# Kernel optimization log

Hardware: AMD Instinct MI355X
Metric: run time of the kernel (lower is better)

## Reference

```python
import jax, jax.numpy as jnp
import numpy as np

NEG = -1e10  # the original uses -10000000000.0
B, T, L = 64, 512, 64
START, END = 0, L - 1


def setup_inputs() -> dict:
    key = jax.random.key(0)
    k_em, k_tr, k_len = jax.random.split(key, 3)
    emission_scores = jax.random.normal(k_em, (B, T, L), dtype=jnp.float32)
    # transition initialized as in __init__: randn with start column / end row masked
    transition = jax.random.normal(k_tr, (L, L), dtype=jnp.float32)
    transition = transition.at[:, START].set(NEG)
    transition = transition.at[END, :].set(NEG)
    sent_lens = jax.random.randint(k_len, (B,), T // 2, T + 1, dtype=jnp.int32)
    return {"emission_scores": emission_scores, "transition": transition,
            "sent_lens": sent_lens}


def reference(emission_scores, transition, sent_lens):
    # --- calculate_all_scores ---
    em = emission_scores.at[:, :, START].set(NEG).at[:, :, END].set(NEG)
    # scores[b,t,y_prev,y_t] = transition[y_prev,y_t] + emission[b,t,y_t]
    scores = transition[None, None, :, :] + em[:, :, None, :]  # [B,T,L,L]
    scores = scores.at[:, 1:, START, :].set(NEG)

    # --- forward_score: sequential DP via scan ---
    alpha0 = scores[:, 0, START, :]  # [B,L]

    def step(alpha_prev, s_t):  # s_t: [B,L,L]
        alpha_t = jax.nn.logsumexp(alpha_prev[:, :, None] + s_t, axis=1)
        return alpha_t, alpha_t

    _, alphas_rest = jax.lax.scan(step, alpha0, jnp.moveaxis(scores[:, 1:], 1, 0))
    alpha = jnp.concatenate([alpha0[:, None, :], jnp.moveaxis(alphas_rest, 0, 1)],
                            axis=1)  # [B,T,L]

    idx = (sent_lens - 1).astype(jnp.int32)[:, None, None]  # [B,1,1]
    last_alpha = jnp.take_along_axis(alpha, idx, axis=1)[:, 0, :]  # [B,L]
    last_alpha = last_alpha + transition[:, END][None, :]
    log_Z = jax.nn.logsumexp(last_alpha, axis=1)  # [B]
    return alpha, log_Z
```

## Files before the change

kernel.cpp:

```cpp
#include <hip/hip_runtime.h>

#define NEGV -10000000000.0f
constexpr int Bn = 64, Tn = 512, Ln = 64;
constexpr int CK = 32;
constexpr int NC = 16;
constexpr int QP = 68;

typedef float f32x16 __attribute__((ext_vector_type(16)));
typedef __bf16 bf16x8 __attribute__((ext_vector_type(8)));
typedef unsigned int u32;
typedef unsigned short u16;

__device__ inline float waveMaxF(float v) {
#pragma unroll
    for (int off = 32; off > 0; off >>= 1)
        v = fmaxf(v, __shfl_xor(v, off, 64));
    return v;
}
__device__ inline u32 packbf(float a, float b) {
    u32 ua = __float_as_uint(a) + 0x8000u;
    u32 ub = __float_as_uint(b) + 0x8000u;
    return (ua >> 16) | (ub & 0xffff0000u);
}
__device__ inline float lo16f(u32 d) { return __uint_as_float(d << 16); }
__device__ inline float hi16f(u32 d) { return __uint_as_float(d & 0xffff0000u); }

template <bool FIRST>
__device__ void chunk_scan(const float* __restrict__ emb, const float* __restrict__ tr,
                           float* __restrict__ outb, float* uLDS,
                           const float* Ecol,
                           float entry,
                           int t0, int j, int len, float* aLastOut, float trSj) {
    const bool edge = (j == 0) || (j == Ln - 1);
    float emq[4];
#pragma unroll
    for (int tt = 0; tt < 4; ++tt) {
        float v = emb[(t0 + tt) * Ln + j];
        emq[tt] = edge ? NEGV : v;
    }
    float aPrev, mPrev, u;
    int tauStart;
    if (FIRST) {
        float a0 = trSj + emq[0];
        outb[t0 * Ln + j] = a0;
        aPrev = a0;
        mPrev = __shfl(a0, 1, 64);
        u = __expf(a0 - mPrev);
        tauStart = 1;
    } else {
        aPrev = entry;
        mPrev = __shfl(entry, 1, 64);
        u = __expf(entry - mPrev);
        tauStart = 0;
    }
    float aLast = *aLastOut;
#pragma unroll 4
    for (int tau = tauStart; tau < CK; ++tau) {
        const int t = t0 + tau;
        uLDS[j] = u;
        const float em_t = emq[tau & 3];
        const int tp = tau + 4;
        if (tp < CK) {
            float v = emb[(t0 + tp) * Ln + j];
            emq[tp & 3] = edge ? NEGV : v;
        }
        float mNext = __shfl(aPrev, 1, 64);
        float cf = __expf(em_t + (mPrev - mNext));
        float acc0 = 0.f, acc1 = 0.f, acc2 = 0.f, acc3 = 0.f;
        const float4* u4 = reinterpret_cast<const float4*>(uLDS);
#pragma unroll
        for (int i4 = 0; i4 < 16; ++i4) {
            float4 uv = u4[i4];
            acc0 = fmaf(uv.x, Ecol[4 * i4 + 0], acc0);
            acc1 = fmaf(uv.y, Ecol[4 * i4 + 1], acc1);
            acc2 = fmaf(uv.z, Ecol[4 * i4 + 2], acc2);
            acc3 = fmaf(uv.w, Ecol[4 * i4 + 3], acc3);
        }
        float S = (acc0 + acc1) + (acc2 + acc3);
        float lg = __logf(S);
        lg = (S > 0.f) ? lg : NEGV;
        float a_t = em_t + (mPrev + lg);
        outb[t * Ln + j] = a_t;
        if (t == len - 1) aLast = a_t;
        u = S * cf;
        aPrev = a_t;
        mPrev = mNext;
    }
    *aLastOut = aLast;
    uLDS[j] = aPrev;
}

__global__ __launch_bounds__(64) void crf_passA(const float* __restrict__ em,
                                                const float* __restrict__ tr,
                                                float* __restrict__ out,
                                                float* __restrict__ wsE,
                                                float* __restrict__ wsS) {
    const int b = blockIdx.x & 63;
    const int cix = blockIdx.x >> 6;
    const int L = threadIdx.x;
    __shared__ alignas(16) float gtab[CK * 64];
    __shared__ alignas(16) u16 Qlds[64 * QP];
    __shared__ alignas(16) float uLDS[64];

    if (cix == 0) {
        float Ecol[Ln];
#pragma unroll
        for (int i = 0; i < Ln; ++i) Ecol[i] = __expf(tr[i * Ln + L]);
        const float trSj = tr[L];
        const float* emb = em + (size_t)b * Tn * Ln;
        float* outb = out + (size_t)b * Tn * Ln;
        float dummyLast = 0.f;
        chunk_scan<true>(emb, tr, outb, uLDS, Ecol, 0.f, 0, L,  -12345, &dummyLast, trSj);
        wsE[b * 1024 + 1 * 64 + L] = uLDS[L];
        return;
    }

    const int t0 = CK * cix;
    const int h = L >> 5;
    const int c31 = L & 31;

    float sSum = 0.f;
#pragma unroll 4
    for (int tau = 0; tau < CK; ++tau) {
        float v = em[((size_t)b * Tn + (t0 + tau)) * Ln + L];
        if (L == 0 || L == Ln - 1) v = NEGV;
        float s = waveMaxF(v);
        gtab[tau * 64 + L] = __expf(v - s);
        sSum += s;
    }

    uint4 Ap[2][4];
#pragma unroll
    for (int I = 0; I < 2; ++I)
#pragma unroll
        for (int kc = 0; kc < 4; ++kc) {
            float e[8];
#pragma unroll
            for (int q = 0; q < 8; ++q) {
                int k = 16 * kc + 8 * h + q;
                e[q] = __expf(tr[k * Ln + 32 * I + c31]);
            }
            Ap[I][kc] = make_uint4(packbf(e[0], e[1]), packbf(e[2], e[3]),
                                   packbf(e[4], e[5]), packbf(e[6], e[7]));
        }

    float mxPrev;
    {
        float mx0 = 0.f;
#pragma unroll
        for (int k4 = 0; k4 < 16; ++k4) {
            float v0 = __expf(tr[L * Ln + 4 * k4 + 0]) * gtab[4 * k4 + 0];
            float v1 = __expf(tr[L * Ln + 4 * k4 + 1]) * gtab[4 * k4 + 1];
            float v2 = __expf(tr[L * Ln + 4 * k4 + 2]) * gtab[4 * k4 + 2];
            float v3 = __expf(tr[L * Ln + 4 * k4 + 3]) * gtab[4 * k4 + 3];
            mx0 = fmaxf(mx0, fmaxf(fmaxf(v0, v1), fmaxf(v2, v3)));
            uint2 w;
            w.x = packbf(v0, v1);
            w.y = packbf(v2, v3);
            *(uint2*)&Qlds[L * QP + 4 * k4] = w;
        }
        mxPrev = waveMaxF(mx0);
    }
    float sigma = sSum;
    const f32x16 Z = (f32x16)(0.0f);

    for (int tau = 1; tau < CK; ++tau) {
        uint4 Bp[2][4];
#pragma unroll
        for (int J = 0; J < 2; ++J)
#pragma unroll
            for (int kc = 0; kc < 4; ++kc) {
                const u16* p = &Qlds[(32 * J + c31) * QP + 16 * kc + 8 * h];
                uint2 q0 = *(const uint2*)(p);
                uint2 q1 = *(const uint2*)(p + 4);
                Bp[J][kc] = make_uint4(q0.x, q0.y, q1.x, q1.y);
            }
        f32x16 acc[2][2];
#pragma unroll
        for (int I = 0; I < 2; ++I)
#pragma unroll
            for (int J = 0; J < 2; ++J) {
                f32x16 a = Z;
#pragma unroll
                for (int kc = 0; kc < 4; ++kc)
                    a = __builtin_amdgcn_mfma_f32_32x32x16_bf16(
                        __builtin_bit_cast(bf16x8, Ap[I][kc]),
                        __builtin_bit_cast(bf16x8, Bp[J][kc]), a, 0, 0, 0);
                acc[I][J] = a;
            }
        float rho = 1.0f / mxPrev;
        sigma += __logf(mxPrev);
        float nmx = 0.f;
#pragma unroll
        for (int I = 0; I < 2; ++I)
#pragma unroll
            for (int rg = 0; rg < 4; ++rg) {
                int k0 = 32 * I + 8 * rg + 4 * h;
                float4 G = *(const float4*)&gtab[tau * 64 + k0];
                float g0 = G.x * rho, g1 = G.y * rho, g2 = G.z * rho, g3 = G.w * rho;
#pragma unroll
                for (int J = 0; J < 2; ++J) {
                    float v0 = acc[I][J][4 * rg + 0] * g0;
                    float v1 = acc[I][J][4 * rg + 1] * g1;
                    float v2 = acc[I][J][4 * rg + 2] * g2;
                    float v3 = acc[I][J][4 * rg + 3] * g3;
                    nmx = fmaxf(nmx, fmaxf(fmaxf(v0, v1), fmaxf(v2, v3)));
                    uint2 w;
                    w.x = packbf(v0, v1);
                    w.y = packbf(v2, v3);
                    *(uint2*)&Qlds[(32 * J + c31) * QP + k0] = w;
                }
            }
        mxPrev = waveMaxF(nmx);
    }

    {
        float rv[64];
        float rmax = 0.f;
#pragma unroll
        for (int n = 0; n < 64; ++n) {
            float v = __uint_as_float(((u32)Qlds[n * QP + L]) << 16);
            rv[n] = v;
            rmax = fmaxf(rmax, v);
        }
        float inv = (rmax > 0.f) ? 1.0f / rmax : 0.f;
        float sj = (rmax > 0.f) ? sigma + __logf(rmax) : 0.f;
        u32* og = (u32*)out + (size_t)b * (Tn * Ln) + (size_t)cix * (CK * Ln) + L * 32;
#pragma unroll
        for (int w8 = 0; w8 < 8; ++w8) {
            uint4 w;
            w.x = packbf(rv[8 * w8 + 0] * inv, rv[8 * w8 + 1] * inv);
            w.y = packbf(rv[8 * w8 + 2] * inv, rv[8 * w8 + 3] * inv);
            w.z = packbf(rv[8 * w8 + 4] * inv, rv[8 * w8 + 5] * inv);
            w.w = packbf(rv[8 * w8 + 6] * inv, rv[8 * w8 + 7] * inv);
            *(uint4*)(og + 4 * w8) = w;
        }
        wsS[b * 1024 + cix * 64 + L] = sj;
    }
}

__global__ __launch_bounds__(64) void crf_passB(const float* __restrict__ out,
                                                float* __restrict__ wsE,
                                                const float* __restrict__ wsS) {
    const int b = blockIdx.x;
    const int j = threadIdx.x;
    __shared__ alignas(16) float uL[64];
    const u32* Qbase = (const u32*)out + (size_t)b * (Tn * Ln);

    float e = wsE[b * 1024 + 1 * 64 + j];
    uint4 nxt[8];
    float signxt = wsS[b * 1024 + 1 * 64 + j];
#pragma unroll
    for (int r = 0; r < 8; ++r) nxt[r] = *(const uint4*)(Qbase + 1 * (CK * Ln) + j * 32 + 4 * r);

#pragma unroll
    for (int c = 1; c <= 14; ++c) {
        uint4 cur[8];
#pragma unroll
        for (int r = 0; r < 8; ++r) cur[r] = nxt[r];
        float sig = signxt;
        if (c < 14) {
#pragma unroll
            for (int r = 0; r < 8; ++r)
                nxt[r] = *(const uint4*)(Qbase + (size_t)(c + 1) * (CK * Ln) + j * 32 + 4 * r);
            signxt = wsS[b * 1024 + (c + 1) * 64 + j];
        }
        float m = __shfl(e, 1, 64);
        uL[j] = __expf(e - m);
        const float4* u4 = reinterpret_cast<const float4*>(uL);
        float S = 0.f;
#pragma unroll
        for (int i4 = 0; i4 < 16; ++i4) {
            float4 uv = u4[i4];
            u32 d0 = ((const u32*)cur)[2 * i4];
            u32 d1 = ((const u32*)cur)[2 * i4 + 1];
            S = fmaf(uv.x, lo16f(d0), S);
            S = fmaf(uv.y, hi16f(d0), S);
            S = fmaf(uv.z, lo16f(d1), S);
            S = fmaf(uv.w, hi16f(d1), S);
        }
        float a;
        if (S > 0.f) a = m + sig + __logf(S);
        else a = m + NEGV + ((j == 0) ? NEGV : 0.f);
        e = a;
        wsE[b * 1024 + (c + 1) * 64 + j] = e;
    }
}

__global__ __launch_bounds__(64) void crf_passC(const float* __restrict__ em,
                                                const float* __restrict__ tr,
                                                const int* __restrict__ lens,
                                                float* __restrict__ out,
                                                const float* __restrict__ wsE) {
    const int b = blockIdx.x & 63;
    const int cix = 1 + (blockIdx.x >> 6);
    const int j = threadIdx.x;
    __shared__ alignas(16) float uLDS[64];

    float Ecol[Ln];
#pragma unroll
    for (int i = 0; i < Ln; ++i) Ecol[i] = __expf(tr[i * Ln + j]);
    const float trEj = tr[j * Ln + (Ln - 1)];
    const int len = lens[b];
    const float* emb = em + (size_t)b * Tn * Ln;
    float* outb = out + (size_t)b * Tn * Ln;
    const float entry = wsE[b * 1024 + cix * 64 + j];

    float aLast = 0.f;
    chunk_scan<false>(emb, tr, outb, uLDS, Ecol, entry, CK * cix, j, len, &aLast, 0.f);

    if (((len - 1) >> 5) == cix) {
        float last = aLast + trEj;
        float m2 = last;
#pragma unroll
        for (int off = 32; off > 0; off >>= 1)
            m2 = fmaxf(m2, __shfl_xor(m2, off, 64));
        float e2 = __expf(last - m2);
#pragma unroll
        for (int off = 32; off > 0; off >>= 1)
            e2 += __shfl_xor(e2, off, 64);
        if (j == 0) out[(size_t)Bn * Tn * Ln + b] = m2 + __logf(e2);
    }
}

__global__ __launch_bounds__(64) void crf_fallback(const float* __restrict__ em,
                                                   const float* __restrict__ tr,
                                                   const int* __restrict__ lens,
                                                   float* __restrict__ out) {
    const int b = blockIdx.x;
    const int j = threadIdx.x;
    __shared__ alignas(16) float uLDS[Ln];
    float E[Ln];
#pragma unroll
    for (int i = 0; i < Ln; ++i) E[i] = __expf(tr[i * Ln + j]);
    const float trSj = tr[j];
    const float trEj = tr[j * Ln + (Ln - 1)];
    const int len = lens[b];
    const bool edge = (j == 0) || (j == Ln - 1);
    const float* emb = em + (size_t)b * Tn * Ln;
    float* outb = out + (size_t)b * Tn * Ln;
    float emq[4];
#pragma unroll
    for (int tt = 0; tt < 4; ++tt) {
        float v = emb[tt * Ln + j];
        emq[tt] = edge ? NEGV : v;
    }
    float a = trSj + emq[0];
    outb[j] = a;
    float aPrev = a, aLast = a;
    float mPrev = __shfl(a, 1, 64);
    float u = __expf(a - mPrev);
#pragma unroll 4
    for (int t = 1; t < Tn; ++t) {
        uLDS[j] = u;
        const float em_t = emq[t & 3];
        const int tp = t + 4;
        if (tp < Tn) {
            float v = emb[tp * Ln + j];
            emq[tp & 3] = edge ? NEGV : v;
        }
        float mNext = __shfl(aPrev, 1, 64);
        float cf = __expf(em_t + (mPrev - mNext));
        float acc0 = 0.f, acc1 = 0.f, acc2 = 0.f, acc3 = 0.f;
        const float4* u4 = reinterpret_cast<const float4*>(uLDS);
#pragma unroll
        for (int i4 = 0; i4 < 16; ++i4) {
            float4 uv = u4[i4];
            acc0 = fmaf(uv.x, E[4 * i4 + 0], acc0);
            acc1 = fmaf(uv.y, E[4 * i4 + 1], acc1);
            acc2 = fmaf(uv.z, E[4 * i4 + 2], acc2);
            acc3 = fmaf(uv.w, E[4 * i4 + 3], acc3);
        }
        float S = (acc0 + acc1) + (acc2 + acc3);
        float lg = __logf(S);
        lg = (S > 0.f) ? lg : NEGV;
        float a_t = em_t + (mPrev + lg);
        outb[t * Ln + j] = a_t;
        if (t == len - 1) aLast = a_t;
        u = S * cf;
        aPrev = a_t;
        mPrev = mNext;
    }
    float last = aLast + trEj;
    float m2 = last;
#pragma unroll
    for (int off = 32; off > 0; off >>= 1)
        m2 = fmaxf(m2, __shfl_xor(m2, off, 64));
    float e2 = __expf(last - m2);
#pragma unroll
    for (int off = 32; off > 0; off >>= 1)
        e2 += __shfl_xor(e2, off, 64);
    if (j == 0) out[(size_t)Bn * Tn * Ln + b] = m2 + __logf(e2);
}

extern "C" void kernel_launch(void* const* d_in, const int* in_sizes, int n_in,
                              void* d_out, int out_size, void* d_ws, size_t ws_size,
                              hipStream_t stream) {
    const float* em = (const float*)d_in[0];
    const float* tr = (const float*)d_in[1];
    const int* lens = (const int*)d_in[2];
    float* out = (float*)d_out;
    const size_t wsNeed = 2u * 64 * 16 * 64 * sizeof(float);
    if (ws_size >= wsNeed) {
        float* wsE = (float*)d_ws;
        float* wsS = wsE + 64 * 16 * 64;
        crf_passA<<<dim3(1024), dim3(64), 0, stream>>>(em, tr, out, wsE, wsS);
        crf_passB<<<dim3(64), dim3(64), 0, stream>>>(out, wsE, wsS);
        crf_passC<<<dim3(960), dim3(64), 0, stream>>>(em, tr, lens, out, wsE);
    } else {
        crf_fallback<<<dim3(Bn), dim3(64), 0, stream>>>(em, tr, lens, out);
    }
}
```

Before: 143.3 us.

## Split passA chunk matrix product across two waves with lazy rescaling

crf_passA now runs with 128 threads. Each wave owns one 32-column half of the chunk transfer matrix, so each wave issues half the MFMAs per step and the serial chain per block gets shorter. The per-timestep wave max and renormalization now run only every fourth step, with separate per-wave scale accumulators reconciled at the end through LDS. The emission max reductions are batched across 16 timesteps to expose more ILP. The cost is an extra wave per block, two barriers, and a risk of bf16 range growth between rescales.

```diff
diff --git a/kernel.cpp b/kernel.cpp
--- a/kernel.cpp
+++ b/kernel.cpp
@@ -26,11 +26,10 @@
 __device__ inline float hi16f(u32 d) { return __uint_as_float(d & 0xffff0000u); }
 
 template <bool FIRST>
-__device__ void chunk_scan(const float* __restrict__ emb, const float* __restrict__ tr,
+__device__ void chunk_scan(const float* __restrict__ emb,
                            float* __restrict__ outb, float* uLDS,
-                           const float* Ecol,
-                           float entry,
-                           int t0, int j, int len, float* aLastOut, float trSj) {
+                           const float* Ecol, float entry, int t0, int j, int len,
+                           float trSj, float* aLastOut, float* aFinalOut) {
     const bool edge = (j == 0) || (j == Ln - 1);
     float emq[4];
 #pragma unroll
@@ -87,47 +86,68 @@
         mPrev = mNext;
     }
     *aLastOut = aLast;
-    uLDS[j] = aPrev;
-}
-
-__global__ __launch_bounds__(64) void crf_passA(const float* __restrict__ em,
-                                                const float* __restrict__ tr,
-                                                float* __restrict__ out,
-                                                float* __restrict__ wsE,
-                                                float* __restrict__ wsS) {
+    *aFinalOut = aPrev;
+}
+
+__global__ __launch_bounds__(128) void crf_passA(const float* __restrict__ em,
+                                                 const float* __restrict__ tr,
+                                                 float* __restrict__ out,
+                                                 float* __restrict__ wsE,
+                                                 float* __restrict__ wsS) {
     const int b = blockIdx.x & 63;
     const int cix = blockIdx.x >> 6;
-    const int L = threadIdx.x;
+    const int J = threadIdx.x >> 6;
+    const int L = threadIdx.x & 63;
     __shared__ alignas(16) float gtab[CK * 64];
     __shared__ alignas(16) u16 Qlds[64 * QP];
     __shared__ alignas(16) float uLDS[64];
+    __shared__ float sLDS[2];
+    __shared__ float sigLDS[2];
 
     if (cix == 0) {
+        if (J == 1) return;
         float Ecol[Ln];
 #pragma unroll
         for (int i = 0; i < Ln; ++i) Ecol[i] = __expf(tr[i * Ln + L]);
         const float trSj = tr[L];
         const float* emb = em + (size_t)b * Tn * Ln;
         float* outb = out + (size_t)b * Tn * Ln;
-        float dummyLast = 0.f;
-        chunk_scan<true>(emb, tr, outb, uLDS, Ecol, 0.f, 0, L,  -12345, &dummyLast, trSj);
-        wsE[b * 1024 + 1 * 64 + L] = uLDS[L];
+        float dummyLast = 0.f, aFinal;
+        chunk_scan<true>(emb, outb, uLDS, Ecol, 0.f, 0, L,  -1, trSj, &dummyLast, &aFinal);
+        wsE[b * 1024 + 1 * 64 + L] = aFinal;
         return;
     }
 
     const int t0 = CK * cix;
+    const int c31 = L & 31;
     const int h = L >> 5;
-    const int c31 = L & 31;
-
-    float sSum = 0.f;
-#pragma unroll 4
-    for (int tau = 0; tau < CK; ++tau) {
-        float v = em[((size_t)b * Tn + (t0 + tau)) * Ln + L];
-        if (L == 0 || L == Ln - 1) v = NEGV;
-        float s = waveMaxF(v);
-        gtab[tau * 64 + L] = __expf(v - s);
-        sSum += s;
-    }
+
+    {
+        float orig[16], sv[16];
+        const int tb = t0 + 16 * J;
+#pragma unroll
+        for (int r = 0; r < 16; ++r) {
+            float v = em[((size_t)b * Tn + (tb + r)) * Ln + L];
+            if (L == 0 || L == Ln - 1) v = NEGV;
+            orig[r] = v;
+            sv[r] = v;
+        }
+#pragma unroll
+        for (int off = 32; off > 0; off >>= 1) {
+#pragma unroll
+            for (int r = 0; r < 16; ++r)
+                sv[r] = fmaxf(sv[r], __shfl_xor(sv[r], off, 64));
+        }
+        float ssum = 0.f;
+#pragma unroll
+        for (int r = 0; r < 16; ++r) {
+            gtab[(16 * J + r) * 64 + L] = __expf(orig[r] - sv[r]);
+            ssum += sv[r];
+        }
+        if (L == 0) sLDS[J] = ssum;
+    }
+    __syncthreads();
+    const float sSum = sLDS[0] + sLDS[1];
 
     uint4 Ap[2][4];
 #pragma unroll
@@ -144,99 +164,101 @@
                                    packbf(e[4], e[5]), packbf(e[6], e[7]));
         }
 
-    float mxPrev;
+    const int n = 32 * J + c31;
     {
-        float mx0 = 0.f;
-#pragma unroll
-        for (int k4 = 0; k4 < 16; ++k4) {
-            float v0 = __expf(tr[L * Ln + 4 * k4 + 0]) * gtab[4 * k4 + 0];
-            float v1 = __expf(tr[L * Ln + 4 * k4 + 1]) * gtab[4 * k4 + 1];
-            float v2 = __expf(tr[L * Ln + 4 * k4 + 2]) * gtab[4 * k4 + 2];
-            float v3 = __expf(tr[L * Ln + 4 * k4 + 3]) * gtab[4 * k4 + 3];
-            mx0 = fmaxf(mx0, fmaxf(fmaxf(v0, v1), fmaxf(v2, v3)));
+        const float* trn = tr + n * Ln + 32 * h;
+        const float* g0 = gtab + 32 * h;
+#pragma unroll
+        for (int k4 = 0; k4 < 8; ++k4) {
+            float v0 = __expf(trn[4 * k4 + 0]) * g0[4 * k4 + 0];
+            float v1 = __expf(trn[4 * k4 + 1]) * g0[4 * k4 + 1];
+            float v2 = __expf(trn[4 * k4 + 2]) * g0[4 * k4 + 2];
+            float v3 = __expf(trn[4 * k4 + 3]) * g0[4 * k4 + 3];
             uint2 w;
             w.x = packbf(v0, v1);
             w.y = packbf(v2, v3);
-            *(uint2*)&Qlds[L * QP + 4 * k4] = w;
-        }
-        mxPrev = waveMaxF(mx0);
-    }
-    float sigma = sSum;
+            *(uint2*)&Qlds[n * QP + 32 * h + 4 * k4] = w;
+        }
+    }
+
+    float sig_w = 0.f;
+    float wm = 1.0f;
     const f32x16 Z = (f32x16)(0.0f);
-
     for (int tau = 1; tau < CK; ++tau) {
-        uint4 Bp[2][4];
-#pragma unroll
-        for (int J = 0; J < 2; ++J)
-#pragma unroll
-            for (int kc = 0; kc < 4; ++kc) {
-                const u16* p = &Qlds[(32 * J + c31) * QP + 16 * kc + 8 * h];
-                uint2 q0 = *(const uint2*)(p);
-                uint2 q1 = *(const uint2*)(p + 4);
-                Bp[J][kc] = make_uint4(q0.x, q0.y, q1.x, q1.y);
+        uint4 Bp[4];
+#pragma unroll
+        for (int kc = 0; kc < 4; ++kc) {
+            const u16* p = &Qlds[n * QP + 16 * kc + 8 * h];
+            uint2 q0 = *(const uint2*)(p);
+            uint2 q1 = *(const uint2*)(p + 4);
+            Bp[kc] = make_uint4(q0.x, q0.y, q1.x, q1.y);
+        }
+        f32x16 acc0 = Z, acc1 = Z;
+#pragma unroll
+        for (int kc = 0; kc < 4; ++kc) {
+            acc0 = __builtin_amdgcn_mfma_f32_32x32x16_bf16(
+                __builtin_bit_cast(bf16x8, Ap[0][kc]),
+                __builtin_bit_cast(bf16x8, Bp[kc]), acc0, 0, 0, 0);
+            acc1 = __builtin_amdgcn_mfma_f32_32x32x16_bf16(
+                __builtin_bit_cast(bf16x8, Ap[1][kc]),
+                __builtin_bit_cast(bf16x8, Bp[kc]), acc1, 0, 0, 0);
+        }
+        const bool doRescale = ((tau & 3) == 0);
+        const bool doMeasure = ((tau & 3) == 2);
+        float rr = 1.0f;
+        if (doRescale) {
+            rr = 1.0f / wm;
+            sig_w += __logf(wm);
+        }
+        float lmax = 0.f;
+#pragma unroll
+        for (int I = 0; I < 2; ++I) {
+#pragma unroll
+            for (int rg = 0; rg < 4; ++rg) {
+                const int k0 = 32 * I + 8 * rg + 4 * h;
+                float4 G = *(const float4*)&gtab[tau * 64 + k0];
+                float v0 = (I ? acc1 : acc0)[4 * rg + 0] * (G.x * rr);
+                float v1 = (I ? acc1 : acc0)[4 * rg + 1] * (G.y * rr);
+                float v2 = (I ? acc1 : acc0)[4 * rg + 2] * (G.z * rr);
+                float v3 = (I ? acc1 : acc0)[4 * rg + 3] * (G.w * rr);
+                if (doMeasure) lmax = fmaxf(lmax, fmaxf(fmaxf(v0, v1), fmaxf(v2, v3)));
+                uint2 w;
+                w.x = packbf(v0, v1);
+                w.y = packbf(v2, v3);
+                *(uint2*)&Qlds[n * QP + k0] = w;
             }
-        f32x16 acc[2][2];
-#pragma unroll
-        for (int I = 0; I < 2; ++I)
-#pragma unroll
-            for (int J = 0; J < 2; ++J) {
-                f32x16 a = Z;
-#pragma unroll
-                for (int kc = 0; kc < 4; ++kc)
-                    a = __builtin_amdgcn_mfma_f32_32x32x16_bf16(
-                        __builtin_bit_cast(bf16x8, Ap[I][kc]),
-                        __builtin_bit_cast(bf16x8, Bp[J][kc]), a, 0, 0, 0);
-                acc[I][J] = a;
-            }
-        float rho = 1.0f / mxPrev;
-        sigma += __logf(mxPrev);
-        float nmx = 0.f;
-#pragma unroll
-        for (int I = 0; I < 2; ++I)
-#pragma unroll
-            for (int rg = 0; rg < 4; ++rg) {
-                int k0 = 32 * I + 8 * rg + 4 * h;
-                float4 G = *(const float4*)&gtab[tau * 64 + k0];
-                float g0 = G.x * rho, g1 = G.y * rho, g2 = G.z * rho, g3 = G.w * rho;
-#pragma unroll
-                for (int J = 0; J < 2; ++J) {
-                    float v0 = acc[I][J][4 * rg + 0] * g0;
-                    float v1 = acc[I][J][4 * rg + 1] * g1;
-                    float v2 = acc[I][J][4 * rg + 2] * g2;
-                    float v3 = acc[I][J][4 * rg + 3] * g3;
-                    nmx = fmaxf(nmx, fmaxf(fmaxf(v0, v1), fmaxf(v2, v3)));
-                    uint2 w;
-                    w.x = packbf(v0, v1);
-                    w.y = packbf(v2, v3);
-                    *(uint2*)&Qlds[(32 * J + c31) * QP + k0] = w;
-                }
-            }
-        mxPrev = waveMaxF(nmx);
-    }
-
-    {
-        float rv[64];
-        float rmax = 0.f;
-#pragma unroll
-        for (int n = 0; n < 64; ++n) {
-            float v = __uint_as_float(((u32)Qlds[n * QP + L]) << 16);
-            rv[n] = v;
-            rmax = fmaxf(rmax, v);
-        }
-        float inv = (rmax > 0.f) ? 1.0f / rmax : 0.f;
-        float sj = (rmax > 0.f) ? sigma + __logf(rmax) : 0.f;
-        u32* og = (u32*)out + (size_t)b * (Tn * Ln) + (size_t)cix * (CK * Ln) + L * 32;
-#pragma unroll
-        for (int w8 = 0; w8 < 8; ++w8) {
-            uint4 w;
-            w.x = packbf(rv[8 * w8 + 0] * inv, rv[8 * w8 + 1] * inv);
-            w.y = packbf(rv[8 * w8 + 2] * inv, rv[8 * w8 + 3] * inv);
-            w.z = packbf(rv[8 * w8 + 4] * inv, rv[8 * w8 + 5] * inv);
-            w.w = packbf(rv[8 * w8 + 6] * inv, rv[8 * w8 + 7] * inv);
-            *(uint4*)(og + 4 * w8) = w;
-        }
-        wsS[b * 1024 + cix * 64 + L] = sj;
-    }
+        }
+        if (doMeasure) wm = waveMaxF(lmax);
+    }
+
+    if (L == 0) sigLDS[J] = sSum + sig_w;
+    __syncthreads();
+    const float sg0 = sigLDS[0], sg1 = sigLDS[1];
+    const float smax = fmaxf(sg0, sg1);
+    const float fh = __expf((h ? sg1 : sg0) - smax);
+    const int r = 32 * J + c31;
+    float rv[32];
+    float lmaxr = 0.f;
+#pragma unroll
+    for (int i = 0; i < 32; ++i) {
+        float v = __uint_as_float(((u32)Qlds[(32 * h + i) * QP + r]) << 16) * fh;
+        rv[i] = v;
+        lmaxr = fmaxf(lmaxr, v);
+    }
+    float rmax = fmaxf(lmaxr, __shfl_xor(lmaxr, 32, 64));
+    float inv = (rmax > 0.f) ? 1.0f / rmax : 0.f;
+    float sj = (rmax > 0.f) ? smax + __logf(rmax) : 0.f;
+    u32* og = (u32*)out + (size_t)b * (Tn * Ln) + (size_t)cix * (CK * Ln) + r * 32 + h * 16;
+#pragma unroll
+    for (int w8 = 0; w8 < 4; ++w8) {
+        uint4 w;
+        w.x = packbf(rv[8 * w8 + 0] * inv, rv[8 * w8 + 1] * inv);
+        w.y = packbf(rv[8 * w8 + 2] * inv, rv[8 * w8 + 3] * inv);
+        w.z = packbf(rv[8 * w8 + 4] * inv, rv[8 * w8 + 5] * inv);
+        w.w = packbf(rv[8 * w8 + 6] * inv, rv[8 * w8 + 7] * inv);
+        *(uint4*)(og + 4 * w8) = w;
+    }
+    if (h == 0) wsS[b * 1024 + cix * 64 + r] = sj;
 }
 
 __global__ __launch_bounds__(64) void crf_passB(const float* __restrict__ out,
@@ -306,8 +328,8 @@
     float* outb = out + (size_t)b * Tn * Ln;
     const float entry = wsE[b * 1024 + cix * 64 + j];
 
-    float aLast = 0.f;
-    chunk_scan<false>(emb, tr, outb, uLDS, Ecol, entry, CK * cix, j, len, &aLast, 0.f);
+    float aLast = 0.f, aFinal;
+    chunk_scan<false>(emb, outb, uLDS, Ecol, entry, CK * cix, j, len, 0.f, &aLast, &aFinal);
 
     if (((len - 1) >> 5) == cix) {
         float last = aLast + trEj;
@@ -404,7 +426,7 @@
     if (ws_size >= wsNeed) {
         float* wsE = (float*)d_ws;
         float* wsS = wsE + 64 * 16 * 64;
-        crf_passA<<<dim3(1024), dim3(64), 0, stream>>>(em, tr, out, wsE, wsS);
+        crf_passA<<<dim3(1024), dim3(128), 0, stream>>>(em, tr, out, wsE, wsS);
         crf_passB<<<dim3(64), dim3(64), 0, stream>>>(out, wsE, wsS);
         crf_passC<<<dim3(960), dim3(64), 0, stream>>>(em, tr, lens, out, wsE);
     } else {
```

Result: faster. 134.8 us (-5.9%).
